# Performance work log

Measured on AMD Instinct MI355X. Metric: run time of the kernel, lower is better.

Reference implementation:

```python
import jax, jax.numpy as jnp
import numpy as np

BLOCK = 32  # GGUF Q8_0 block size
O, I = 4096, 4096
NB = I // BLOCK  # blocks per output row
B, S = 2, 2048


def setup_inputs() -> dict:
    key = jax.random.key(0)
    k1, k2, k3, k4 = jax.random.split(key, 4)
    x = jax.random.normal(k1, (B, S, I), dtype=jnp.float32)
    # signed int8 quants stored as int32 (values in [-128, 127])
    q_weight = jax.random.randint(k2, (O, I), 0, 256, dtype=jnp.int32) - 128
    # per-block fp scales (small positive, as produced by Q8_0 quantization)
    scales = jax.random.uniform(k3, (O, NB), dtype=jnp.float32) * 0.02 + 1e-4
    bias = jax.random.normal(k4, (O,), dtype=jnp.float32)
    return {"x": x, "q_weight": q_weight, "scales": scales, "bias": bias}


def dequantize(q_weight, scales, dtype):
    # q_weight: [O, I] int, scales: [O, NB] float; block-wise dequant (Q8_0)
    q = q_weight.reshape(O, NB, BLOCK).astype(dtype)
    w = q * scales.astype(dtype)[:, :, None]
    return w.reshape(O, I)  # [O, I]


def reference(x, q_weight, scales, bias):
    # cast_bias_weight: dequantize weight/bias to the input dtype, then linear
    dtype = x.dtype
    w = dequantize(q_weight, scales, dtype)          # [O, I]
    y = jnp.einsum('bsi,oi->bso', x, w) + bias.astype(dtype)
    return y
```

## Files before the change

kernel.cpp:

```cpp
#include <hip/hip_runtime.h>
#include <hip/hip_bf16.h>
#include <stdint.h>


#define M_DIM 4096
#define N_DIM 4096
#define K_DIM 4096
#define NB_SC 128

#define BM 256
#define BN 256
#define BKB 128
#define NT (K_DIM / BKB)
#define TILE_B (BM * BKB)

typedef __attribute__((ext_vector_type(4))) int i32x4;

__device__ __forceinline__ void gload_lds16(const void* gsrc, void* ldsdst) {
  __builtin_amdgcn_global_load_lds(
      (__attribute__((address_space(1))) void*)(uintptr_t)gsrc,
      (__attribute__((address_space(3))) void*)(uint32_t)(uintptr_t)ldsdst,
      16, 0, 0);
}

__device__ __forceinline__ int pack4(int a, int b, int c, int d) {
  return (a & 255) | ((b & 255) << 8) | ((c & 255) << 16) | ((d & 255) << 24);
}


__global__ void prep_kernel(const float* __restrict__ x, const int* __restrict__ q,
                            const float* __restrict__ sc,
                            char* __restrict__ xb, char* __restrict__ wb,
                            float* __restrict__ sxv, float* __restrict__ swv) {
  __shared__ float red[4];
  const int b = blockIdx.x;
  const int t = threadIdx.x;
  if (b < 4096) {
    const float4* row = (const float4*)(x + (size_t)b * K_DIM);
    float4 v[4];
    float m = 0.f;
#pragma unroll
    for (int i = 0; i < 4; ++i) {
      v[i] = row[t * 4 + i];
      m = fmaxf(m, fmaxf(fmaxf(fabsf(v[i].x), fabsf(v[i].y)),
                         fmaxf(fabsf(v[i].z), fabsf(v[i].w))));
    }
#pragma unroll
    for (int off = 32; off >= 1; off >>= 1) m = fmaxf(m, __shfl_xor(m, off, 64));
    if ((t & 63) == 0) red[t >> 6] = m;
    __syncthreads();
    m = fmaxf(fmaxf(red[0], red[1]), fmaxf(red[2], red[3]));
    const float inv = (m > 0.f) ? 127.0f / m : 0.f;
    int4 o;
    o.x = pack4(__float2int_rn(v[0].x * inv), __float2int_rn(v[0].y * inv),
                __float2int_rn(v[0].z * inv), __float2int_rn(v[0].w * inv));
    o.y = pack4(__float2int_rn(v[1].x * inv), __float2int_rn(v[1].y * inv),
                __float2int_rn(v[1].z * inv), __float2int_rn(v[1].w * inv));
    o.z = pack4(__float2int_rn(v[2].x * inv), __float2int_rn(v[2].y * inv),
                __float2int_rn(v[2].z * inv), __float2int_rn(v[2].w * inv));
    o.w = pack4(__float2int_rn(v[3].x * inv), __float2int_rn(v[3].y * inv),
                __float2int_rn(v[3].z * inv), __float2int_rn(v[3].w * inv));
    ((int4*)(xb + (size_t)b * K_DIM))[t] = o;
    if (t == 0) sxv[b] = m / 127.0f;
  } else {
    const int o_row = b - 4096;
    float m = sc[o_row * NB_SC + (t & 127)];
#pragma unroll
    for (int off = 32; off >= 1; off >>= 1) m = fmaxf(m, __shfl_xor(m, off, 64));
    if ((t & 63) == 0) red[t >> 6] = m;
    __syncthreads();
    m = fmaxf(fmaxf(red[0], red[1]), fmaxf(red[2], red[3]));
    const float ratio = sc[o_row * NB_SC + (t >> 1)] / m;
    const int4* qp = (const int4*)(q + (size_t)o_row * K_DIM);
    int4 qv[4];
#pragma unroll
    for (int i = 0; i < 4; ++i) qv[i] = qp[t * 4 + i];
    int4 ov;
    ov.x = pack4(__float2int_rn((float)qv[0].x * ratio), __float2int_rn((float)qv[0].y * ratio),
                 __float2int_rn((float)qv[0].z * ratio), __float2int_rn((float)qv[0].w * ratio));
    ov.y = pack4(__float2int_rn((float)qv[1].x * ratio), __float2int_rn((float)qv[1].y * ratio),
                 __float2int_rn((float)qv[1].z * ratio), __float2int_rn((float)qv[1].w * ratio));
    ov.z = pack4(__float2int_rn((float)qv[2].x * ratio), __float2int_rn((float)qv[2].y * ratio),
                 __float2int_rn((float)qv[2].z * ratio), __float2int_rn((float)qv[2].w * ratio));
    ov.w = pack4(__float2int_rn((float)qv[3].x * ratio), __float2int_rn((float)qv[3].y * ratio),
                 __float2int_rn((float)qv[3].z * ratio), __float2int_rn((float)qv[3].w * ratio));
    ((int4*)(wb + (size_t)o_row * K_DIM))[t] = ov;
    if (t == 0) swv[o_row] = m;
  }
}


__device__ __forceinline__ void stage_half(const char* __restrict__ pX,
                                           char* lds, int hr0, int ktb, int w) {
#pragma unroll
  for (int j = 0; j < 2; ++j) {
    gload_lds16(pX + (size_t)(hr0 + j * 8) * K_DIM + ktb,
                lds + (hr0 + w * 16 + j * 8) * BKB);
  }
}

template <int BUF, int Q>
__device__ __forceinline__ void read_aq(const char* pa0, const char* pa1,
                                        i32x4 (&af)[2][2]) {
#pragma unroll
  for (int j = 0; j < 2; ++j) {
    af[j][0] = *(const i32x4*)(pa0 + BUF * TILE_B + (Q * 32 + j * 16) * BKB);
    af[j][1] = *(const i32x4*)(pa1 + BUF * TILE_B + (Q * 32 + j * 16) * BKB);
  }
}

template <int BUF>
__device__ __forceinline__ void read_ball(const char* pb0, const char* pb1,
                                          i32x4 (&bf)[4][2]) {
#pragma unroll
  for (int ni = 0; ni < 4; ++ni) {
    bf[ni][0] = *(const i32x4*)(pb0 + BUF * TILE_B + ni * 16 * BKB);
    bf[ni][1] = *(const i32x4*)(pb1 + BUF * TILE_B + ni * 16 * BKB);
  }
}

__device__ __forceinline__ void mfma_quad(const i32x4 (&af)[2][2], const i32x4 (&bf)[4][2],
                                          i32x4 (&acc)[8][4], int q0) {
  __builtin_amdgcn_s_setprio(1);
#pragma unroll
  for (int q = 0; q < 2; ++q)
#pragma unroll
    for (int ni = 0; ni < 4; ++ni)
#pragma unroll
      for (int kk = 0; kk < 2; ++kk)
        acc[q0 + q][ni] =
            __builtin_amdgcn_mfma_i32_16x16x64_i8(af[q][kk], bf[ni][kk], acc[q0 + q][ni], 0, 0, 0);
  __builtin_amdgcn_s_setprio(0);
}

#define PHASE_SYNC()                                   \
  __builtin_amdgcn_s_barrier();                        \
  asm volatile("s_waitcnt lgkmcnt(0)" ::: "memory");   \
  __builtin_amdgcn_sched_barrier(0)

template <int BUF, int MODE>
__device__ __forceinline__ void ktile(const char* pa0, const char* pa1,
                                      const char* pb0, const char* pb1,
                                      const char* __restrict__ pA,
                                      const char* __restrict__ pB,
                                      char* AsB, char* BsB,
                                      int ktb, int w,
                                      i32x4 (&acc)[8][4]) {
  char* Anw = AsB + (BUF ^ 1) * TILE_B;
  char* Aw  = AsB + BUF * TILE_B;
  char* Bw  = BsB + BUF * TILE_B;

  i32x4 bf[4][2];

  {
    i32x4 a0[2][2];
    read_ball<BUF>(pb0, pb1, bf);
    read_aq<BUF, 0>(pa0, pa1, a0);
    if (MODE < 2) stage_half(pA, Anw, 128, ktb + BKB, w);
    asm volatile("s_waitcnt lgkmcnt(8)" ::: "memory");
    PHASE_SYNC();
    mfma_quad(a0, bf, acc, 0);
    __builtin_amdgcn_s_barrier();
  }
  {
    i32x4 a1[2][2];
    read_aq<BUF, 1>(pa0, pa1, a1);
    if (MODE == 0) stage_half(pB, Bw, 0, ktb + 2 * BKB, w);
    PHASE_SYNC();
    mfma_quad(a1, bf, acc, 2);
    __builtin_amdgcn_s_barrier();
  }
  {
    i32x4 a2[2][2];
    read_aq<BUF, 2>(pa0, pa1, a2);
    if (MODE == 0) stage_half(pB, Bw, 128, ktb + 2 * BKB, w);
    PHASE_SYNC();
    mfma_quad(a2, bf, acc, 4);
    __builtin_amdgcn_s_barrier();
  }
  {
    i32x4 a3[2][2];
    read_aq<BUF, 3>(pa0, pa1, a3);
    if (MODE == 0) stage_half(pA, Aw, 0, ktb + 2 * BKB, w);
    PHASE_SYNC();
    mfma_quad(a3, bf, acc, 6);
    if (MODE == 0)
      asm volatile("s_waitcnt vmcnt(6)" ::: "memory");
    else if (MODE == 1)
      asm volatile("s_waitcnt vmcnt(0)" ::: "memory");
    __builtin_amdgcn_s_barrier();
  }
}

__global__ __launch_bounds__(512, 2) void gemm256(const char* __restrict__ A,
                                                  const char* __restrict__ B,
                                                  const float* __restrict__ sxv,
                                                  const float* __restrict__ swv,
                                                  const float* __restrict__ bias,
                                                  float* __restrict__ C) {
  __shared__ char AsB[2 * TILE_B];
  __shared__ char BsB[2 * TILE_B];

  const int tid = threadIdx.x;
  const int w = tid >> 6;
  const int l = tid & 63;
  const int wm = w >> 2;
  const int wn = w & 3;
  const int frow = l & 15;
  const int fkb = (l >> 4) * 16;

  const int bid = blockIdx.x;
  const int cpx = gridDim.x >> 3;
  const int swz = (bid & 7) * cpx + (bid >> 3);
  const int bm0 = (swz >> 4) * BM;
  const int bn0 = (swz & 15) * BN;

  const int fr7 = frow & 7;
  const int sw0 = (((fkb) >> 4) ^ fr7) << 4;
  const int sw1 = (((fkb + 64) >> 4) ^ fr7) << 4;
  const char* pa0 = (const char*)AsB + (wm * 128 + frow) * BKB + sw0;
  const char* pa1 = (const char*)AsB + (wm * 128 + frow) * BKB + sw1;
  const char* pb0 = (const char*)BsB + (wn * 64 + frow) * BKB + sw0;
  const char* pb1 = (const char*)BsB + (wn * 64 + frow) * BKB + sw1;

  const int sr = l >> 3;
  const int skp = ((l & 7) ^ sr) << 4;
  const char* pA = A + (size_t)(bm0 + w * 16 + sr) * K_DIM + skp;
  const char* pB = B + (size_t)(bn0 + w * 16 + sr) * K_DIM + skp;

  i32x4 acc[8][4] = {};

  stage_half(pB, BsB, 0, 0, w);
  stage_half(pB, BsB, 128, 0, w);
  stage_half(pA, AsB, 0, 0, w);
  stage_half(pA, AsB, 128, 0, w);
  stage_half(pB, BsB + TILE_B, 0, BKB, w);
  stage_half(pB, BsB + TILE_B, 128, BKB, w);
  stage_half(pA, AsB + TILE_B, 0, BKB, w);
  asm volatile("s_waitcnt vmcnt(6)" ::: "memory");
  __builtin_amdgcn_s_barrier();

  for (int t = 0; t < NT - 2; t += 2) {
    ktile<0, 0>(pa0, pa1, pb0, pb1, pA, pB, AsB, BsB, t * BKB, w, acc);
    ktile<1, 0>(pa0, pa1, pb0, pb1, pA, pB, AsB, BsB, (t + 1) * BKB, w, acc);
  }
  ktile<0, 1>(pa0, pa1, pb0, pb1, pA, pB, AsB, BsB, (NT - 2) * BKB, w, acc);
  ktile<1, 2>(pa0, pa1, pb0, pb1, pA, pB, AsB, BsB, (NT - 1) * BKB, w, acc);

#pragma unroll
  for (int ni = 0; ni < 4; ++ni) {
    const int n = bn0 + wn * 64 + ni * 16 + (l & 15);
    const float swn = swv[n];
    const float bv = bias[n];
#pragma unroll
    for (int mi = 0; mi < 8; ++mi) {
      const int mbase = bm0 + wm * 128 + mi * 16 + (l >> 4) * 4;
#pragma unroll
      for (int r = 0; r < 4; ++r)
        C[(size_t)(mbase + r) * N_DIM + n] =
            (float)acc[mi][ni][r] * (swn * sxv[mbase + r]) + bv;
    }
  }
}


__global__ void naive_kernel(const float* __restrict__ x, const int* __restrict__ q,
                             const float* __restrict__ sc, const float* __restrict__ bias,
                             float* __restrict__ out) {
  size_t idx = (size_t)blockIdx.x * blockDim.x + threadIdx.x;
  if (idx >= (size_t)M_DIM * N_DIM) return;
  int n = (int)(idx & (N_DIM - 1));
  size_t m = idx >> 12;
  float acc = 0.f;
  for (int k = 0; k < K_DIM; k += 32) {
    float s = sc[n * NB_SC + (k >> 5)];
    float part = 0.f;
    for (int j = 0; j < 32; ++j)
      part += x[m * K_DIM + k + j] * (float)q[(size_t)n * K_DIM + k + j];
    acc += part * s;
  }
  out[idx] = acc + bias[n];
}


extern "C" void kernel_launch(void* const* d_in, const int* in_sizes, int n_in,
                              void* d_out, int out_size, void* d_ws, size_t ws_size,
                              hipStream_t stream) {
  const float* x    = (const float*)d_in[0];
  const int*   q    = (const int*)d_in[1];
  const float* sc   = (const float*)d_in[2];
  const float* bias = (const float*)d_in[3];
  float* out = (float*)d_out;

  const size_t elems = (size_t)M_DIM * K_DIM;
  const size_t need  = 2 * elems + 2 * 4096 * sizeof(float);

  if (ws_size >= need) {
    char* xb = (char*)d_ws;
    char* wb = xb + elems;
    float* sxv = (float*)(wb + elems);
    float* swv = sxv + 4096;
    hipLaunchKernelGGL(prep_kernel, dim3(8192), dim3(256), 0, stream,
                       x, q, sc, xb, wb, sxv, swv);
    hipLaunchKernelGGL(gemm256, dim3((M_DIM / BM) * (N_DIM / BN)), dim3(512), 0, stream,
                       xb, wb, sxv, swv, bias, out);
  } else {
    hipLaunchKernelGGL(naive_kernel, dim3((M_DIM * N_DIM) / 256), dim3(256), 0, stream,
                       x, q, sc, bias, out);
  }
}
```

Baseline: 94.64 us.

## Triple-buffer B tiles and collapse per-phase barriers to one per k-tile

B gets a third LDS buffer, and each k-tile issues all its global-to-LDS staging up front. The four LDS-read plus MFMA phases then run without intermediate barriers, with a single wait and barrier at the end of the tile. The main loop is unrolled by six so the buffer indices (A mod 2, B mod 3) stay compile-time constants. The aim is to cut barrier and synchronisation stalls inside the MFMA stream, at the cost of using the full LDS budget and giving the compiler less explicit interleaving control.

```diff
diff --git a/kernel.cpp b/kernel.cpp
--- a/kernel.cpp
+++ b/kernel.cpp
@@ -133,12 +133,7 @@
   __builtin_amdgcn_s_setprio(0);
 }
 
-#define PHASE_SYNC()                                   \
-  __builtin_amdgcn_s_barrier();                        \
-  asm volatile("s_waitcnt lgkmcnt(0)" ::: "memory");   \
-  __builtin_amdgcn_sched_barrier(0)
-
-template <int BUF, int MODE>
+template <int AB, int BB, int MODE>
 __device__ __forceinline__ void ktile(const char* pa0, const char* pa1,
                                       const char* pb0, const char* pb1,
                                       const char* __restrict__ pA,
@@ -146,49 +141,38 @@
                                       char* AsB, char* BsB,
                                       int ktb, int w,
                                       i32x4 (&acc)[8][4]) {
-  char* Anw = AsB + (BUF ^ 1) * TILE_B;
-  char* Aw  = AsB + BUF * TILE_B;
-  char* Bw  = BsB + BUF * TILE_B;
+  char* An = AsB + (AB ^ 1) * TILE_B;
+  char* Bw = BsB + ((BB + 2) % 3) * TILE_B;
+
+  if (MODE < 2) {
+    stage_half(pA, An, 0, ktb + BKB, w);
+    stage_half(pA, An, 128, ktb + BKB, w);
+  }
+  if (MODE == 0) {
+    stage_half(pB, Bw, 0, ktb + 2 * BKB, w);
+    stage_half(pB, Bw, 128, ktb + 2 * BKB, w);
+  }
 
   i32x4 bf[4][2];
-
-  {
-    i32x4 a0[2][2];
-    read_ball<BUF>(pb0, pb1, bf);
-    read_aq<BUF, 0>(pa0, pa1, a0);
-    if (MODE < 2) stage_half(pA, Anw, 128, ktb + BKB, w);
-    asm volatile("s_waitcnt lgkmcnt(8)" ::: "memory");
-    PHASE_SYNC();
-    mfma_quad(a0, bf, acc, 0);
-    __builtin_amdgcn_s_barrier();
-  }
-  {
-    i32x4 a1[2][2];
-    read_aq<BUF, 1>(pa0, pa1, a1);
-    if (MODE == 0) stage_half(pB, Bw, 0, ktb + 2 * BKB, w);
-    PHASE_SYNC();
-    mfma_quad(a1, bf, acc, 2);
-    __builtin_amdgcn_s_barrier();
-  }
-  {
-    i32x4 a2[2][2];
-    read_aq<BUF, 2>(pa0, pa1, a2);
-    if (MODE == 0) stage_half(pB, Bw, 128, ktb + 2 * BKB, w);
-    PHASE_SYNC();
-    mfma_quad(a2, bf, acc, 4);
-    __builtin_amdgcn_s_barrier();
-  }
-  {
-    i32x4 a3[2][2];
-    read_aq<BUF, 3>(pa0, pa1, a3);
-    if (MODE == 0) stage_half(pA, Aw, 0, ktb + 2 * BKB, w);
-    PHASE_SYNC();
-    mfma_quad(a3, bf, acc, 6);
+  i32x4 a0[2][2], a1[2][2], a2[2][2], a3[2][2];
+  read_ball<BB>(pb0, pb1, bf);
+  read_aq<AB, 0>(pa0, pa1, a0);
+  mfma_quad(a0, bf, acc, 0);
+  read_aq<AB, 1>(pa0, pa1, a1);
+  mfma_quad(a1, bf, acc, 2);
+  read_aq<AB, 2>(pa0, pa1, a2);
+  mfma_quad(a2, bf, acc, 4);
+  read_aq<AB, 3>(pa0, pa1, a3);
+  mfma_quad(a3, bf, acc, 6);
+
+  if (MODE < 2) {
+    asm volatile("s_waitcnt lgkmcnt(0)" ::: "memory");
     if (MODE == 0)
-      asm volatile("s_waitcnt vmcnt(6)" ::: "memory");
-    else if (MODE == 1)
+      asm volatile("s_waitcnt vmcnt(4)" ::: "memory");
+    else
       asm volatile("s_waitcnt vmcnt(0)" ::: "memory");
     __builtin_amdgcn_s_barrier();
+    __builtin_amdgcn_sched_barrier(0);
   }
 }
 
@@ -199,7 +183,7 @@
                                                   const float* __restrict__ bias,
                                                   float* __restrict__ C) {
   __shared__ char AsB[2 * TILE_B];
-  __shared__ char BsB[2 * TILE_B];
+  __shared__ char BsB[3 * TILE_B];
 
   const int tid = threadIdx.x;
   const int w = tid >> 6;
@@ -230,22 +214,25 @@
 
   i32x4 acc[8][4] = {};
 
+  stage_half(pA, AsB, 0, 0, w);
+  stage_half(pA, AsB, 128, 0, w);
   stage_half(pB, BsB, 0, 0, w);
   stage_half(pB, BsB, 128, 0, w);
-  stage_half(pA, AsB, 0, 0, w);
-  stage_half(pA, AsB, 128, 0, w);
   stage_half(pB, BsB + TILE_B, 0, BKB, w);
   stage_half(pB, BsB + TILE_B, 128, BKB, w);
-  stage_half(pA, AsB + TILE_B, 0, BKB, w);
-  asm volatile("s_waitcnt vmcnt(6)" ::: "memory");
+  asm volatile("s_waitcnt vmcnt(4)" ::: "memory");
   __builtin_amdgcn_s_barrier();
 
-  for (int t = 0; t < NT - 2; t += 2) {
-    ktile<0, 0>(pa0, pa1, pb0, pb1, pA, pB, AsB, BsB, t * BKB, w, acc);
-    ktile<1, 0>(pa0, pa1, pb0, pb1, pA, pB, AsB, BsB, (t + 1) * BKB, w, acc);
-  }
-  ktile<0, 1>(pa0, pa1, pb0, pb1, pA, pB, AsB, BsB, (NT - 2) * BKB, w, acc);
-  ktile<1, 2>(pa0, pa1, pb0, pb1, pA, pB, AsB, BsB, (NT - 1) * BKB, w, acc);
+  for (int t = 0; t < NT - 2; t += 6) {
+    ktile<0, 0, 0>(pa0, pa1, pb0, pb1, pA, pB, AsB, BsB, (t + 0) * BKB, w, acc);
+    ktile<1, 1, 0>(pa0, pa1, pb0, pb1, pA, pB, AsB, BsB, (t + 1) * BKB, w, acc);
+    ktile<0, 2, 0>(pa0, pa1, pb0, pb1, pA, pB, AsB, BsB, (t + 2) * BKB, w, acc);
+    ktile<1, 0, 0>(pa0, pa1, pb0, pb1, pA, pB, AsB, BsB, (t + 3) * BKB, w, acc);
+    ktile<0, 1, 0>(pa0, pa1, pb0, pb1, pA, pB, AsB, BsB, (t + 4) * BKB, w, acc);
+    ktile<1, 2, 0>(pa0, pa1, pb0, pb1, pA, pB, AsB, BsB, (t + 5) * BKB, w, acc);
+  }
+  ktile<0, 0, 1>(pa0, pa1, pb0, pb1, pA, pB, AsB, BsB, (NT - 2) * BKB, w, acc);
+  ktile<1, 1, 2>(pa0, pa1, pb0, pb1, pA, pB, AsB, BsB, (NT - 1) * BKB, w, acc);
 
 #pragma unroll
   for (int ni = 0; ni < 4; ++ni) {
```

New measurement: 92.65 us. -2.1%, faster.
